# Performance work log

Hardware: AMD Instinct MI355X
Metric: run time of the kernel (lower is better)

The kernel has to match this reference:

```python
import jax, jax.numpy as jnp
import numpy as np

DIM, HEADS = 512, 8
HD = DIM // HEADS            # 64
WS = (8, 8)                  # window_size
DS = (2, 2)                  # dilated_size
TW = (WS[0] * DS[0], WS[1] * DS[1])  # total_window_size = (16,16)
SHIFT = (4, 4)


def _rope_tables():
    # Axial 2D RoPE over the (Wh, Ww) window grid: first half of head_dim
    # encodes the h coordinate, second half the w coordinate.
    da = HD // 2
    inv = 1.0 / (10000.0 ** (np.arange(0, da, 2) / da))        # (da/2,)
    ah = np.arange(WS[0])[:, None] * inv                        # (Wh, da/2)
    aw = np.arange(WS[1])[:, None] * inv                        # (Ww, da/2)
    ang = np.concatenate([
        np.broadcast_to(ah[:, None, :], (WS[0], WS[1], da // 2)),
        np.broadcast_to(aw[None, :, :], (WS[0], WS[1], da // 2)),
    ], axis=-1)                                                 # (Wh, Ww, HD/2)
    return jnp.asarray(np.cos(ang), jnp.float32), jnp.asarray(np.sin(ang), jnp.float32)


def _apply_rope(x, cos, sin):
    # x: (M, Wh, Ww, HD); rotate consecutive pairs
    xr = x.reshape(*x.shape[:-1], HD // 2, 2)
    x1, x2 = xr[..., 0], xr[..., 1]
    out = jnp.stack([x1 * cos - x2 * sin, x1 * sin + x2 * cos], axis=-1)
    return out.reshape(x.shape)


def _attn_mask(H, W):
    # Faithful to create_mask (incl. the quirky w_slices where slice(-8,0) is
    # empty and slice(0,None) overwrites the whole row band).
    img = np.zeros((H, W), np.float32)
    cnt = 0
    for hs in (slice(0, -WS[0]), slice(-WS[0], -SHIFT[0]), slice(-SHIFT[0], None)):
        for wsl in (slice(0, -WS[1]), slice(-WS[1], 0), slice(0, None)):
            img[hs, wsl] = cnt
            cnt += 1
    th, tw = TW
    m = img.reshape(H // th, th, W // tw, tw).transpose(0, 2, 1, 3).reshape(-1, th, tw)
    nW = m.shape[0]
    dh, dw = DS
    m = m.reshape(nW, th // dh, dh, tw // dw, dw).transpose(0, 1, 3, 2, 4)
    m = m.reshape(nW, -1, dh * dw).transpose(0, 2, 1).reshape(nW * dh * dw, -1)  # (nW*4, 64)
    diff = m[:, None, :] - m[:, :, None]
    return jnp.asarray(np.where(diff != 0, -1e9, 0.0).astype(np.float32))


def _windows(t):
    # roll -> total-window partition -> dilated partition (Swin-style)
    B, H, W, C = t.shape
    t = jnp.roll(t, (-SHIFT[0], -SHIFT[1]), axis=(1, 2))
    th, tw = TW
    t = t.reshape(B, H // th, th, W // tw, tw, C).transpose(0, 1, 3, 2, 4, 5).reshape(-1, th, tw, C)
    Bw = t.shape[0]                                            # B * nW
    dh, dw = DS
    t = t.reshape(Bw, th // dh, dh, tw // dw, dw, C).transpose(0, 1, 3, 2, 4, 5)
    t = t.reshape(Bw, -1, dh * dw, C).transpose(0, 2, 1, 3).reshape(Bw * dh * dw, -1, C)
    return t, Bw                                               # (Bw*4, 64, C)


def setup_inputs() -> dict:
    key = jax.random.key(0)
    ks = jax.random.split(key, 8)
    B, H, W, C = 4, 128, 128, DIM
    s = 0.02
    return {
        "x": jax.random.normal(ks[0], (B, H, W, C), jnp.float32),
        "cross": jax.random.normal(ks[1], (B, H, W, C), jnp.float32),
        "qv_w": jax.random.normal(ks[2], (C, 2 * C), jnp.float32) * s,
        "qv_b": jnp.zeros((2 * C,), jnp.float32),
        "k_w": jax.random.normal(ks[3], (C, C), jnp.float32) * s,
        "k_b": jnp.zeros((C,), jnp.float32),
        "proj_w": jax.random.normal(ks[4], (C, C), jnp.float32) * s,
        "proj_b": jnp.zeros((C,), jnp.float32),
    }


def reference(x, cross, qv_w, qv_b, k_w, k_b, proj_w, proj_b):
    B, H, W, C = x.shape
    scale = HD ** -0.5
    xw, Bw = _windows(x)
    cw, _ = _windows(cross)
    B_, N, _ = xw.shape                                        # N = 64
    qv = (xw @ qv_w + qv_b).reshape(B_, N, 2, HEADS, HD).transpose(2, 0, 3, 1, 4)
    q, v = qv[0], qv[1]                                        # (B_, h, N, HD)
    k = (cw @ k_w + k_b).reshape(B_, N, HEADS, HD).transpose(0, 2, 1, 3)
    cos, sin = _rope_tables()
    q = _apply_rope(q.reshape(-1, WS[0], WS[1], HD), cos, sin).reshape(B_, HEADS, N, HD)
    k = _apply_rope(k.reshape(-1, WS[0], WS[1], HD), cos, sin).reshape(B_, HEADS, N, HD)
    attn = jnp.einsum('bhnd,bhmd->bhnm', q * scale, k)
    mask = _attn_mask(H, W)                                    # (nW*4, N, N)
    nWd = mask.shape[0]
    attn = attn.reshape(B_ // nWd, nWd, HEADS, N, N) + mask[None, :, None]
    attn = jax.nn.softmax(attn, axis=-1).reshape(B_, HEADS, N, N)
    out = jnp.einsum('bhnm,bhmd->bhnd', attn, v).transpose(0, 2, 1, 3).reshape(B_, N, C)
    # reverse dilation, then reverse total windows, then un-roll
    dh, dw = DS
    th, tw = TW
    out = out.reshape(Bw, dh * dw, N, C).transpose(0, 2, 1, 3).reshape(-1, dh * dw, C)
    out = out.reshape(Bw, th // dh, tw // dw, dh, dw, C).transpose(0, 1, 3, 2, 4, 5).reshape(Bw, th, tw, C)
    out = out.reshape(B, H // th, W // tw, th, tw, C).transpose(0, 1, 3, 2, 4, 5).reshape(B, H, W, C)
    out = jnp.roll(out, (SHIFT[0], SHIFT[1]), axis=(1, 2))
    return out @ proj_w + proj_b
```

## Files before the change

kernel.cpp:

```cpp
#include <hip/hip_runtime.h>


typedef float v4f __attribute__((ext_vector_type(4)));
typedef short short8 __attribute__((ext_vector_type(8)));
typedef unsigned short us4 __attribute__((ext_vector_type(4)));

#define BM 128
#define BN 128

__device__ __forceinline__ unsigned short f2bf(float f) {
  unsigned int u = __builtin_bit_cast(unsigned int, f);
  u += 0x7fffu + ((u >> 16) & 1u);
  return (unsigned short)(u >> 16);
}

__device__ __forceinline__ void gload_lds16(const void* g, void* l) {
  __builtin_amdgcn_global_load_lds((const __attribute__((address_space(1))) void*)g,
                                   (__attribute__((address_space(3))) void*)l, 16, 0, 0);
}

__device__ __forceinline__ int tok2pix(int tok) {
  int g = tok >> 6, n = tok & 63;
  int b = g >> 8, rem = g & 255;
  int d = rem & 3, bw = rem >> 2;
  int wh = bw >> 3, ww = bw & 7;
  int ph = n >> 3, pw = n & 7;
  int ii = (wh * 16 + 2 * ph + (d >> 1) + 4) & 127;
  int jj = (ww * 16 + 2 * pw + (d & 1) + 4) & 127;
  return (b * 128 + ii) * 128 + jj;
}

__global__ __launch_bounds__(256) void prep_kernel(
    const float* __restrict__ qv_w, const float* __restrict__ k_w,
    const float* __restrict__ proj_w,
    unsigned short* __restrict__ qv_wt, unsigned short* __restrict__ k_wt,
    unsigned short* __restrict__ proj_wt,
    float* __restrict__ rope_cos, float* __restrict__ rope_sin) {
  int tid = blockIdx.x * 256 + threadIdx.x;
  if (tid < 524288) {
    int c = tid >> 9, k = tid & 511;
    qv_wt[tid] = f2bf(qv_w[k * 1024 + c]);
  } else if (tid < 786432) {
    int t = tid - 524288;
    int c = t >> 9, k = t & 511;
    k_wt[t] = f2bf(k_w[k * 512 + c]);
  } else if (tid < 1048576) {
    int t = tid - 786432;
    int c = t >> 9, k = t & 511;
    proj_wt[t] = f2bf(proj_w[k * 512 + c]);
  } else if (tid < 1048576 + 2048) {
    int t = tid - 1048576;
    int pos = t >> 5, tt = t & 31;
    int ph = pos >> 3, pw = pos & 7;
    float e = (float)(tt & 15) * (1.0f / 16.0f);
    float inv = powf(10000.0f, -e);
    float ang = (float)(tt < 16 ? ph : pw) * inv;
    rope_cos[t] = cosf(ang);
    rope_sin[t] = sinf(ang);
  }
}

__global__ __launch_bounds__(256) void convert_kernel(
    const float* __restrict__ in, unsigned short* __restrict__ out) {
  unsigned int stride = gridDim.x * 256u;
  for (unsigned int i = blockIdx.x * 256u + threadIdx.x; i < 4194304u; i += stride) {
    size_t e = (size_t)i * 8;
    v4f t0 = *(const v4f*)(in + e);
    v4f t1 = *(const v4f*)(in + e + 4);
    short8 w;
    w[0] = (short)f2bf(t0[0]); w[1] = (short)f2bf(t0[1]);
    w[2] = (short)f2bf(t0[2]); w[3] = (short)f2bf(t0[3]);
    w[4] = (short)f2bf(t1[0]); w[5] = (short)f2bf(t1[1]);
    w[6] = (short)f2bf(t1[2]); w[7] = (short)f2bf(t1[3]);
    *(short8*)(out + e) = w;
  }
}

template <int MODE>
__global__ __launch_bounds__(256) void gemm_kernel(
    const unsigned short* __restrict__ Ap, const unsigned short* __restrict__ Wt,
    const float* __restrict__ bias, void* __restrict__ out0,
    void* __restrict__ out1, const float* __restrict__ rope_cos,
    const float* __restrict__ rope_sin) {
  __shared__ __attribute__((aligned(16))) unsigned short As[4096];
  __shared__ __attribute__((aligned(16))) unsigned short Bs[4096];
  int tid = threadIdx.x;

  constexpr int NBN = (MODE == 0) ? 8 : 4;
  constexpr int NWG = 512 * NBN;
  constexpr int CPX = NWG / 8;
  int lin = blockIdx.x;
  int wgid = (lin & 7) * CPX + (lin >> 3);
  int bm = wgid / NBN;
  int bn = wgid % NBN;

  int lane = tid & 63, wid = tid >> 6;
  int wm = (wid & 1) * 64, wn = (wid >> 1) * 64;
  int l15 = lane & 15, quad = lane >> 4;

  const unsigned short* pa[2];
  const unsigned short* pb[2];
  unsigned short* lA[2];
  unsigned short* lB[2];
#pragma unroll
  for (int i = 0; i < 2; i++) {
    int c = i * 256 + tid;
    int h = c >> 7, row = (c & 127) ^ h;
    int tokA = bm * BM + row;
    size_t arow = (MODE == 2) ? (size_t)tokA : (size_t)tok2pix(tokA);
    pa[i] = Ap + arow * 512 + h * 8;
    pb[i] = Wt + (size_t)(bn * BN + row) * 512 + h * 8;
    lA[i] = As + (size_t)(i * 256 + wid * 64) * 8;
    lB[i] = Bs + (size_t)(i * 256 + wid * 64) * 8;
  }

  v4f acc[4][4];
#pragma unroll
  for (int i = 0; i < 4; i++)
#pragma unroll
    for (int j = 0; j < 4; j++) acc[i][j] = (v4f){0.f, 0.f, 0.f, 0.f};

  for (int k0 = 0; k0 < 512; k0 += 32) {
#pragma unroll
    for (int i = 0; i < 2; i++) {
      gload_lds16(pa[i] + k0, lA[i]);
      gload_lds16(pb[i] + k0, lB[i]);
    }
    __syncthreads();
    short8 af[4], bfr[4];
#pragma unroll
    for (int i = 0; i < 4; i++)
      af[i] = *(const short8*)(As + ((quad * 128 + ((wm + i * 16 + l15) ^ quad)) << 3));
#pragma unroll
    for (int j = 0; j < 4; j++)
      bfr[j] = *(const short8*)(Bs + ((quad * 128 + ((wn + j * 16 + l15) ^ quad)) << 3));
#pragma unroll
    for (int i = 0; i < 4; i++)
#pragma unroll
      for (int j = 0; j < 4; j++)
        acc[i][j] = __builtin_amdgcn_mfma_f32_16x16x32_bf16(af[i], bfr[j], acc[i][j], 0, 0, 0);
    __syncthreads();
  }

#pragma unroll
  for (int j = 0; j < 4; j++) {
    int col = bn * BN + wn + j * 16 + l15;
    float bv = bias[col];
    int which = col >> 9;
    int h = (col >> 6) & 7;
    int hd = col & 63;
#pragma unroll
    for (int i = 0; i < 4; i++) {
      int tok0 = bm * BM + wm + i * 16 + quad * 4;
      if (MODE == 0 && which == 1) {
        int g = tok0 >> 6, n0 = tok0 & 63;
        us4 wv;
#pragma unroll
        for (int r = 0; r < 4; r++) wv[r] = f2bf(acc[i][j][r] + bv);
        *(us4*)((unsigned short*)out1 + ((((g * 8 + h) * 64 + hd) << 6) + n0)) = wv;
      } else if (MODE == 2) {
#pragma unroll
        for (int r = 0; r < 4; r++)
          ((float*)out0)[(size_t)tok2pix(tok0 + r) * 512 + col] = acc[i][j][r] + bv;
      } else {
#pragma unroll
        for (int r = 0; r < 4; r++) {
          int tok = tok0 + r;
          int g = tok >> 6, n = tok & 63;
          float val = acc[i][j][r] + bv;
          float part = __shfl_xor(val, 1);
          int ti = (n << 5) + (hd >> 1);
          float c = rope_cos[ti], s = rope_sin[ti];
          float o = (hd & 1) ? (part * s + val * c) : (val * c - part * s);
          if (MODE == 0) o *= 0.125f;
          ((unsigned short*)out0)[(((g * 8 + h) * 64 + n) << 6) + hd] = f2bf(o);
        }
      }
    }
  }
}

__global__ __launch_bounds__(256) void attn_kernel(
    const unsigned short* __restrict__ Qbuf, const unsigned short* __restrict__ Kbuf,
    const unsigned short* __restrict__ Vbuf, unsigned short* __restrict__ Obuf) {
  __shared__ __attribute__((aligned(16))) unsigned short Ps[4096];
  int bid = blockIdx.x;
  int g = bid >> 3, h = bid & 7;
  int tid = threadIdx.x;
  int lane = tid & 63, w = tid >> 6;
  int l15 = lane & 15, quad = lane >> 4;
  size_t base = ((size_t)(g * 8 + h)) << 12;
  const unsigned short* Q = Qbuf + base;
  const unsigned short* K = Kbuf + base;
  const unsigned short* Vt = Vbuf + base;

  v4f s[4];
#pragma unroll
  for (int j = 0; j < 4; j++) s[j] = (v4f){0.f, 0.f, 0.f, 0.f};
#pragma unroll
  for (int ki = 0; ki < 2; ki++) {
    short8 aq = *(const short8*)(Q + (w * 16 + l15) * 64 + ki * 32 + quad * 8);
#pragma unroll
    for (int j = 0; j < 4; j++) {
      short8 bk = *(const short8*)(K + (j * 16 + l15) * 64 + ki * 32 + quad * 8);
      s[j] = __builtin_amdgcn_mfma_f32_16x16x32_bf16(aq, bk, s[j], 0, 0, 0);
    }
  }

  int rem = g & 255;
  bool masked_win = ((rem >> 5) == 7);
  float p[4][4];
#pragma unroll
  for (int j = 0; j < 4; j++) {
    int m = j * 16 + l15;
    int pm = m >> 3;
    int gm = (int)(pm >= 4) + (int)(pm >= 6);
#pragma unroll
    for (int r = 0; r < 4; r++) {
      int row = w * 16 + quad * 4 + r;
      int pq = row >> 3;
      int gq = (int)(pq >= 4) + (int)(pq >= 6);
      float v = s[j][r];
      if (masked_win && gm != gq) v = -1e9f;
      p[j][r] = v;
    }
  }
#pragma unroll
  for (int r = 0; r < 4; r++) {
    float mx = fmaxf(fmaxf(p[0][r], p[1][r]), fmaxf(p[2][r], p[3][r]));
    mx = fmaxf(mx, __shfl_xor(mx, 1));
    mx = fmaxf(mx, __shfl_xor(mx, 2));
    mx = fmaxf(mx, __shfl_xor(mx, 4));
    mx = fmaxf(mx, __shfl_xor(mx, 8));
    float sum = 0.f;
#pragma unroll
    for (int j = 0; j < 4; j++) { p[j][r] = __expf(p[j][r] - mx); sum += p[j][r]; }
    sum += __shfl_xor(sum, 1);
    sum += __shfl_xor(sum, 2);
    sum += __shfl_xor(sum, 4);
    sum += __shfl_xor(sum, 8);
    float inv = 1.0f / sum;
    int row = w * 16 + quad * 4 + r;
#pragma unroll
    for (int j = 0; j < 4; j++) {
      int m = j * 16 + l15;
      int h8 = m >> 3;
      Ps[((h8 * 64 + (row ^ h8)) << 3) + (m & 7)] = f2bf(p[j][r] * inv);
    }
  }
  __syncthreads();

  v4f o[4];
#pragma unroll
  for (int j = 0; j < 4; j++) o[j] = (v4f){0.f, 0.f, 0.f, 0.f};
#pragma unroll
  for (int ki = 0; ki < 2; ki++) {
    int h8 = ki * 4 + quad;
    short8 ap = *(const short8*)(Ps + ((h8 * 64 + ((w * 16 + l15) ^ h8)) << 3));
#pragma unroll
    for (int j = 0; j < 4; j++) {
      short8 bv = *(const short8*)(Vt + (j * 16 + l15) * 64 + ki * 32 + quad * 8);
      o[j] = __builtin_amdgcn_mfma_f32_16x16x32_bf16(ap, bv, o[j], 0, 0, 0);
    }
  }
#pragma unroll
  for (int j = 0; j < 4; j++) {
    int hd = j * 16 + l15;
#pragma unroll
    for (int r = 0; r < 4; r++) {
      int row = w * 16 + quad * 4 + r;
      Obuf[(size_t)(g * 64 + row) * 512 + h * 64 + hd] = f2bf(o[j][r]);
    }
  }
}

extern "C" void kernel_launch(void* const* d_in, const int* in_sizes, int n_in,
                              void* d_out, int out_size, void* d_ws, size_t ws_size,
                              hipStream_t stream) {
  const float* x      = (const float*)d_in[0];
  const float* cross  = (const float*)d_in[1];
  const float* qv_w   = (const float*)d_in[2];
  const float* qv_b   = (const float*)d_in[3];
  const float* k_w    = (const float*)d_in[4];
  const float* k_b    = (const float*)d_in[5];
  const float* proj_w = (const float*)d_in[6];
  const float* proj_b = (const float*)d_in[7];

  char* ws = (char*)d_ws;
  const size_t MB = 1024 * 1024;
  unsigned short* Qbuf = (unsigned short*)(ws);
  unsigned short* Kbuf = (unsigned short*)(ws + 64 * MB);
  unsigned short* Vbuf = (unsigned short*)(ws + 128 * MB);
  unsigned short* Obuf = (unsigned short*)(ws + 192 * MB);
  unsigned short* qv_wt = (unsigned short*)(ws + 256 * MB);
  unsigned short* k_wt = qv_wt + 1024 * 512;
  unsigned short* proj_wt = k_wt + 512 * 512;
  float* rope_cos = (float*)(proj_wt + 512 * 512);
  float* rope_sin = rope_cos + 2048;
  unsigned short* cvt = Obuf;

  prep_kernel<<<4104, 256, 0, stream>>>(qv_w, k_w, proj_w, qv_wt, k_wt, proj_wt,
                                        rope_cos, rope_sin);
  convert_kernel<<<2048, 256, 0, stream>>>(x, cvt);
  gemm_kernel<0><<<4096, 256, 0, stream>>>(cvt, qv_wt, qv_b, Qbuf, Vbuf,
                                           rope_cos, rope_sin);
  convert_kernel<<<2048, 256, 0, stream>>>(cross, cvt);
  gemm_kernel<1><<<2048, 256, 0, stream>>>(cvt, k_wt, k_b, Kbuf, nullptr,
                                           rope_cos, rope_sin);
  attn_kernel<<<8192, 256, 0, stream>>>(Qbuf, Kbuf, Vbuf, Obuf);
  gemm_kernel<2><<<2048, 256, 0, stream>>>(Obuf, proj_wt, proj_b, d_out, nullptr,
                                           rope_cos, rope_sin);
}
```

Baseline: 782.5 us.

## Double-buffer GEMM LDS tiles and move window gather into convert kernel

The GEMM K-loop now double-buffers its LDS tiles, issuing the global-to-LDS loads for the next K slice before computing on the current one. This halves the number of barriers per iteration and overlaps memory with MFMA. The token-to-pixel window gather moves out of the GEMM A-loads and into the fp32-to-bf16 convert kernel, which now writes a pre-permuted activation buffer, so the GEMM reads A rows contiguously. The costs are doubled LDS usage and a scattered read pattern in the convert kernel. Any other GEMM that reads the converted input, or any MODE that expected raw pixel order, now depends on this reordering.

```diff
diff --git a/kernel.cpp b/kernel.cpp
--- a/kernel.cpp
+++ b/kernel.cpp
@@ -64,15 +64,16 @@
     const float* __restrict__ in, unsigned short* __restrict__ out) {
   unsigned int stride = gridDim.x * 256u;
   for (unsigned int i = blockIdx.x * 256u + threadIdx.x; i < 4194304u; i += stride) {
-    size_t e = (size_t)i * 8;
-    v4f t0 = *(const v4f*)(in + e);
-    v4f t1 = *(const v4f*)(in + e + 4);
+    int tok = (int)(i >> 6), c8 = (int)(i & 63) * 8;
+    size_t src = (size_t)tok2pix(tok) * 512 + c8;
+    v4f t0 = *(const v4f*)(in + src);
+    v4f t1 = *(const v4f*)(in + src + 4);
     short8 w;
     w[0] = (short)f2bf(t0[0]); w[1] = (short)f2bf(t0[1]);
     w[2] = (short)f2bf(t0[2]); w[3] = (short)f2bf(t0[3]);
     w[4] = (short)f2bf(t1[0]); w[5] = (short)f2bf(t1[1]);
     w[6] = (short)f2bf(t1[2]); w[7] = (short)f2bf(t1[3]);
-    *(short8*)(out + e) = w;
+    *(short8*)(out + (size_t)tok * 512 + c8) = w;
   }
 }
 
@@ -82,8 +83,8 @@
     const float* __restrict__ bias, void* __restrict__ out0,
     void* __restrict__ out1, const float* __restrict__ rope_cos,
     const float* __restrict__ rope_sin) {
-  __shared__ __attribute__((aligned(16))) unsigned short As[4096];
-  __shared__ __attribute__((aligned(16))) unsigned short Bs[4096];
+  __shared__ __attribute__((aligned(16))) unsigned short As[2][4096];
+  __shared__ __attribute__((aligned(16))) unsigned short Bs[2][4096];
   int tid = threadIdx.x;
 
   constexpr int NBN = (MODE == 0) ? 8 : 4;
@@ -100,18 +101,14 @@
 
   const unsigned short* pa[2];
   const unsigned short* pb[2];
-  unsigned short* lA[2];
-  unsigned short* lB[2];
+  int lOff[2];
 #pragma unroll
   for (int i = 0; i < 2; i++) {
     int c = i * 256 + tid;
     int h = c >> 7, row = (c & 127) ^ h;
-    int tokA = bm * BM + row;
-    size_t arow = (MODE == 2) ? (size_t)tokA : (size_t)tok2pix(tokA);
-    pa[i] = Ap + arow * 512 + h * 8;
+    pa[i] = Ap + (size_t)(bm * BM + row) * 512 + h * 8;
     pb[i] = Wt + (size_t)(bn * BN + row) * 512 + h * 8;
-    lA[i] = As + (size_t)(i * 256 + wid * 64) * 8;
-    lB[i] = Bs + (size_t)(i * 256 + wid * 64) * 8;
+    lOff[i] = (i * 256 + wid * 64) * 8;
   }
 
   v4f acc[4][4];
@@ -120,26 +117,38 @@
 #pragma unroll
     for (int j = 0; j < 4; j++) acc[i][j] = (v4f){0.f, 0.f, 0.f, 0.f};
 
-  for (int k0 = 0; k0 < 512; k0 += 32) {
-#pragma unroll
-    for (int i = 0; i < 2; i++) {
-      gload_lds16(pa[i] + k0, lA[i]);
-      gload_lds16(pb[i] + k0, lB[i]);
-    }
-    __syncthreads();
+#pragma unroll
+  for (int i = 0; i < 2; i++) {
+    gload_lds16(pa[i], &As[0][lOff[i]]);
+    gload_lds16(pb[i], &Bs[0][lOff[i]]);
+  }
+  __syncthreads();
+
+  int cur = 0;
+  for (int t = 0; t < 16; ++t) {
+    if (t < 15) {
+      int k0 = (t + 1) * 32;
+      int nxt = cur ^ 1;
+#pragma unroll
+      for (int i = 0; i < 2; i++) {
+        gload_lds16(pa[i] + k0, &As[nxt][lOff[i]]);
+        gload_lds16(pb[i] + k0, &Bs[nxt][lOff[i]]);
+      }
+    }
     short8 af[4], bfr[4];
 #pragma unroll
     for (int i = 0; i < 4; i++)
-      af[i] = *(const short8*)(As + ((quad * 128 + ((wm + i * 16 + l15) ^ quad)) << 3));
+      af[i] = *(const short8*)(&As[cur][(quad * 128 + ((wm + i * 16 + l15) ^ quad)) << 3]);
 #pragma unroll
     for (int j = 0; j < 4; j++)
-      bfr[j] = *(const short8*)(Bs + ((quad * 128 + ((wn + j * 16 + l15) ^ quad)) << 3));
+      bfr[j] = *(const short8*)(&Bs[cur][(quad * 128 + ((wn + j * 16 + l15) ^ quad)) << 3]);
 #pragma unroll
     for (int i = 0; i < 4; i++)
 #pragma unroll
       for (int j = 0; j < 4; j++)
         acc[i][j] = __builtin_amdgcn_mfma_f32_16x16x32_bf16(af[i], bfr[j], acc[i][j], 0, 0, 0);
     __syncthreads();
+    cur ^= 1;
   }
 
 #pragma unroll
```

Result: no change. 789.2 us (+0.9%).
